# Kernel optimization log

Measured on AMD Instinct MI355X. Metric: run time of the kernel, lower is better.

The kernel has to match this reference:

```python
import jax, jax.numpy as jnp
import numpy as np

NUM_HEADS = 16
HEAD_DIM = 128  # d_out // num_heads
D_IN = 2048
D_OUT = 2048
B = 2
T = 2048
W_SCALE = 0.02  # keep softmax logits in a sane range


def setup_inputs() -> dict:
    key = jax.random.key(0)
    ks = jax.random.split(key, 6)
    x = jax.random.normal(ks[0], (B, T, D_IN), dtype=jnp.float32)
    Wq = jax.random.normal(ks[1], (D_OUT, D_IN), dtype=jnp.float32) * W_SCALE
    Wk = jax.random.normal(ks[2], (HEAD_DIM, D_IN), dtype=jnp.float32) * W_SCALE
    Wv = jax.random.normal(ks[3], (HEAD_DIM, D_IN), dtype=jnp.float32) * W_SCALE
    Wo = jax.random.normal(ks[4], (D_OUT, D_OUT), dtype=jnp.float32) * W_SCALE
    bo = jnp.zeros((D_OUT,), dtype=jnp.float32)
    return {"x": x, "Wq": Wq, "Wk": Wk, "Wv": Wv, "Wo": Wo, "bo": bo}


def reference(x, Wq, Wk, Wv, Wo, bo):
    b, t, _ = x.shape
    # projections (torch nn.Linear: y = x @ W.T)
    q = jnp.einsum('btd,ed->bte', x, Wq).reshape(b, t, NUM_HEADS, HEAD_DIM)
    q = q.transpose(0, 2, 1, 3)                      # [b, H, T, hd]
    k = jnp.einsum('btd,ed->bte', x, Wk)             # [b, T, hd] single KV head
    v = jnp.einsum('btd,ed->bte', x, Wv)             # [b, T, hd]
    # MQA: single K/V head broadcast across all query heads
    scale = 1.0 / jnp.sqrt(jnp.float32(HEAD_DIM))
    scores = jnp.einsum('bhqd,bkd->bhqk', q, k) * scale  # [b, H, T, T]
    # NOTE: the original module computes a causal mask but never applies it,
    # so attention is unmasked (faithful to source).
    w = jax.nn.softmax(scores, axis=-1)
    ctx = jnp.einsum('bhqk,bkd->bhqd', w, v)         # [b, H, T, hd]
    ctx = ctx.transpose(0, 2, 1, 3).reshape(b, t, D_OUT)
    return jnp.einsum('btd,ed->bte', ctx, Wo) + bo
```

## Files before the change

### kernel.cpp

```cpp
#include <hip/hip_runtime.h>

typedef unsigned short u16;
typedef unsigned int   u32;
typedef __bf16 bf16x8 __attribute__((ext_vector_type(8)));
typedef float  f32x4  __attribute__((ext_vector_type(4)));
typedef u32    u32x2  __attribute__((ext_vector_type(2)));

constexpr int TB   = 2;
constexpr int TT   = 2048;
constexpr int DIN  = 2048;
constexpr int DOUT = 2048;
constexpr int NH   = 16;
constexpr int HD   = 128;
constexpr int MR   = TB * TT;
constexpr int NQKV = DOUT + 2 * HD;

constexpr float QSC = 0.08838834764831845f * 1.4426950408889634f;

__device__ __forceinline__ u16 f2b(float f) {
  return __builtin_bit_cast(u16, (__bf16)f);
}

__global__ __launch_bounds__(256) void k_cast_all(const float* __restrict__ x,
                                                  const float* __restrict__ wq,
                                                  const float* __restrict__ wk,
                                                  const float* __restrict__ wv,
                                                  const float* __restrict__ wo,
                                                  u16* __restrict__ xb,
                                                  u16* __restrict__ wqkv,
                                                  u16* __restrict__ wob) {
  int bid = blockIdx.x;
  const float* s; u16* d; int base;
  if (bid < 8192)       { s = x;  d = xb;   base = bid; }
  else if (bid < 12288) { s = wq; d = wqkv; base = bid - 8192; }
  else if (bid < 12544) { s = wk; d = wqkv + (size_t)DOUT * DIN;        base = bid - 12288; }
  else if (bid < 12800) { s = wv; d = wqkv + (size_t)(DOUT + HD) * DIN; base = bid - 12544; }
  else                  { s = wo; d = wob;  base = bid - 12800; }
  int i = (base * 256 + threadIdx.x) * 4;
  float4 v = *(const float4*)(s + i);
  ushort4 o;
  o.x = f2b(v.x); o.y = f2b(v.y); o.z = f2b(v.z); o.w = f2b(v.w);
  *(ushort4*)(d + i) = o;
}

__device__ __forceinline__ void async16(const u16* g, u16* l) {
  __builtin_amdgcn_global_load_lds((const __attribute__((address_space(1))) void*)g,
                                   (__attribute__((address_space(3))) void*)l,
                                   16, 0, 0);
}

template<bool F32OUT>
__global__ __launch_bounds__(512) void k_gemm(const u16* __restrict__ A,
                                              const u16* __restrict__ Bm,
                                              void* __restrict__ Cv,
                                              const float* __restrict__ bias,
                                              int M, int N, int K) {
  __shared__ u16 lA[128 * 64];
  __shared__ u16 lB[128 * 64];
  const int tid = threadIdx.x;
  const int w = tid >> 6, l = tid & 63;
  const int wr = w >> 1, wc = w & 1;
  const int r16 = l & 15, kq = l >> 4;

  int nwg = gridDim.x * gridDim.y;
  int wg = blockIdx.y * gridDim.x + blockIdx.x;
  if ((nwg & 7) == 0) wg = (wg & 7) * (nwg >> 3) + (wg >> 3);
  const int rowS = (wg / gridDim.x) * 128, colS = (wg % gridDim.x) * 128;

  f32x4 acc[2][4] = {};

  for (int k0 = 0; k0 < K; k0 += 64) {
    __syncthreads();
#pragma unroll
    for (int i = 0; i < 2; ++i) {
      int e = i * 512 + tid;
      int row = e >> 3, col = (e & 7) * 8;
      async16(A  + (size_t)(rowS + row) * K + k0 + col, &lA[e * 8]);
      async16(Bm + (size_t)(colS + row) * K + k0 + col, &lB[e * 8]);
    }
    __syncthreads();
#pragma unroll
    for (int kk = 0; kk < 2; ++kk) {
      bf16x8 af[2], bfr[4];
#pragma unroll
      for (int m = 0; m < 2; ++m)
        af[m] = *(const bf16x8*)&lA[(wr * 32 + m * 16 + r16) * 64 + kk * 32 + kq * 8];
#pragma unroll
      for (int n = 0; n < 4; ++n)
        bfr[n] = *(const bf16x8*)&lB[(wc * 64 + n * 16 + r16) * 64 + kk * 32 + kq * 8];
      __builtin_amdgcn_s_setprio(1);
#pragma unroll
      for (int m = 0; m < 2; ++m)
#pragma unroll
        for (int n = 0; n < 4; ++n)
          acc[m][n] = __builtin_amdgcn_mfma_f32_16x16x32_bf16(af[m], bfr[n], acc[m][n], 0, 0, 0);
      __builtin_amdgcn_s_setprio(0);
    }
  }

#pragma unroll
  for (int m = 0; m < 2; ++m)
#pragma unroll
    for (int n = 0; n < 4; ++n)
#pragma unroll
      for (int j = 0; j < 4; ++j) {
        int r = rowS + wr * 32 + m * 16 + kq * 4 + j;
        int c = colS + wc * 64 + n * 16 + r16;
        if constexpr (F32OUT) {
          ((float*)Cv)[(size_t)r * N + c] = acc[m][n][j] + bias[c];
        } else {
          float v = acc[m][n][j];
          if (c < DOUT) v *= QSC;
          ((u16*)Cv)[(size_t)r * N + c] = f2b(v);
        }
      }
}

__global__ __launch_bounds__(256) void k_transpose_v(const u16* __restrict__ qkv,
                                                     u16* __restrict__ vtg) {
  __shared__ u16 tile[64 * 136];
  const int blk = blockIdx.x;
  const int b = blk / (TT / 64), t0 = (blk % (TT / 64)) * 64;
  const int tid = threadIdx.x;
#pragma unroll
  for (int i = 0; i < 4; ++i) {
    int e = i * 256 + tid;
    int row = e >> 4, col = (e & 15) * 8;
    *(uint4*)&tile[row * 136 + col] =
        *(const uint4*)(qkv + (size_t)(b * TT + t0 + row) * NQKV + DOUT + HD + col);
  }
  __syncthreads();
#pragma unroll
  for (int i = 0; i < 4; ++i) {
    int e = i * 256 + tid;
    int d = e >> 3, tc = (e & 7) * 8;
    u16 tmp[8];
#pragma unroll
    for (int j = 0; j < 8; ++j) tmp[j] = tile[(tc + j) * 136 + d];
    *(uint4*)(vtg + ((size_t)b * HD + d) * TT + t0 + tc) = *(uint4*)tmp;
  }
}

#define KT_IDX(r, c) ((r) * 128 + ((c) ^ (((r) & 7) << 3)))
#define VT_IDX(r, c) ((r) * 64 + ((c) ^ (((r) & 7) << 3)))

__global__ __launch_bounds__(512) void k_attn(const u16* __restrict__ qkv,
                                              const u16* __restrict__ vtg,
                                              u16* __restrict__ ctxg) {
  __shared__ u16 Kt[2][64 * 128];
  __shared__ u16 Vt[2][128 * 64];

  const int qt = blockIdx.x, h = blockIdx.y, b = blockIdx.z;
  const int tid = threadIdx.x, w = tid >> 6, l = tid & 63;
  const int r16 = l & 15, kq = l >> 4;
  const int q0 = qt * 128 + w * 16;
  const size_t rowbase = (size_t)b * TT;

  bf16x8 qf[4];
  const u16* qrow = qkv + (rowbase + q0 + r16) * NQKV + h * HD + kq * 8;
#pragma unroll
  for (int kk = 0; kk < 4; ++kk) qf[kk] = *(const bf16x8*)(qrow + kk * 32);

  const int krow0 = tid >> 4, kcol = (tid & 15) * 8;
  const int vrow0 = tid >> 3, vcol = (tid & 7) * 8;
  const u16* kglob = qkv + (rowbase)*NQKV + DOUT;
  const u16* vglob = vtg + (size_t)b * HD * TT;

  uint4 kr0, kr1, vr0, vr1;
  auto load_tiles = [&](int kv0) {
    const u16* kb = kglob + (size_t)kv0 * NQKV;
    kr0 = *(const uint4*)(kb + (size_t)krow0 * NQKV + kcol);
    kr1 = *(const uint4*)(kb + (size_t)(krow0 + 32) * NQKV + kcol);
    const u16* vb = vglob + kv0;
    vr0 = *(const uint4*)(vb + (size_t)vrow0 * TT + vcol);
    vr1 = *(const uint4*)(vb + (size_t)(vrow0 + 64) * TT + vcol);
  };
  auto write_tiles = [&](int buf) {
    *(uint4*)&Kt[buf][KT_IDX(krow0, kcol)]      = kr0;
    *(uint4*)&Kt[buf][KT_IDX(krow0 + 32, kcol)] = kr1;
    *(uint4*)&Vt[buf][VT_IDX(vrow0, vcol)]      = vr0;
    *(uint4*)&Vt[buf][VT_IDX(vrow0 + 64, vcol)] = vr1;
  };

  f32x4 ctx[8] = {};
  float l_run = 0.0f;

  load_tiles(0);
  write_tiles(0);
  __syncthreads();

  for (int t = 0; t < TT / 64; ++t) {
    const int cur = t & 1;
    if (t < TT / 64 - 1) load_tiles((t + 1) * 64);

    f32x4 s[4] = {};
#pragma unroll
    for (int n = 0; n < 4; ++n) {
      bf16x8 kf[4];
#pragma unroll
      for (int kk = 0; kk < 4; ++kk)
        kf[kk] = *(const bf16x8*)&Kt[cur][KT_IDX(n * 16 + r16, kk * 32 + kq * 8)];
      __builtin_amdgcn_s_setprio(1);
#pragma unroll
      for (int kk = 0; kk < 4; ++kk)
        s[n] = __builtin_amdgcn_mfma_f32_16x16x32_bf16(kf[kk], qf[kk], s[n], 0, 0, 0);
      __builtin_amdgcn_s_setprio(0);
    }

    float rsum = 0.0f;
    float p[4][4];
#pragma unroll
    for (int n = 0; n < 4; ++n)
#pragma unroll
      for (int j = 0; j < 4; ++j) {
        p[n][j] = exp2f(s[n][j]);
        rsum += p[n][j];
      }
    rsum += __shfl_xor(rsum, 16);
    rsum += __shfl_xor(rsum, 32);
    l_run += rsum;

    u32 pk[4][2];
#pragma unroll
    for (int n = 0; n < 4; ++n) {
      pk[n][0] = (u32)f2b(p[n][0]) | ((u32)f2b(p[n][1]) << 16);
      pk[n][1] = (u32)f2b(p[n][2]) | ((u32)f2b(p[n][3]) << 16);
    }

#pragma unroll
    for (int hh = 0; hh < 2; ++hh) {
      union { bf16x8 v; u32 wds[4]; } pu;
      pu.wds[0] = pk[2 * hh][0];     pu.wds[1] = pk[2 * hh][1];
      pu.wds[2] = pk[2 * hh + 1][0]; pu.wds[3] = pk[2 * hh + 1][1];
      __builtin_amdgcn_s_setprio(1);
#pragma unroll
      for (int f = 0; f < 8; ++f) {
        union { bf16x8 v; u32x2 half[2]; } vu;
        vu.half[0] = *(const u32x2*)&Vt[cur][VT_IDX(f * 16 + r16, (2 * hh) * 16 + kq * 4)];
        vu.half[1] = *(const u32x2*)&Vt[cur][VT_IDX(f * 16 + r16, (2 * hh + 1) * 16 + kq * 4)];
        ctx[f] = __builtin_amdgcn_mfma_f32_16x16x32_bf16(vu.v, pu.v, ctx[f], 0, 0, 0);
      }
      __builtin_amdgcn_s_setprio(0);
    }

    if (t < TT / 64 - 1) write_tiles(cur ^ 1);
    __syncthreads();
  }

  const float inv = 1.0f / l_run;
  u16* crow = ctxg + (rowbase + q0 + r16) * DOUT + h * HD + kq * 4;
#pragma unroll
  for (int f = 0; f < 8; ++f) {
    u32x2 o;
    o[0] = (u32)f2b(ctx[f][0] * inv) | ((u32)f2b(ctx[f][1] * inv) << 16);
    o[1] = (u32)f2b(ctx[f][2] * inv) | ((u32)f2b(ctx[f][3] * inv) << 16);
    *(u32x2*)(crow + f * 16) = o;
  }
}

extern "C" void kernel_launch(void* const* d_in, const int* in_sizes, int n_in,
                              void* d_out, int out_size, void* d_ws, size_t ws_size,
                              hipStream_t stream) {
  const float* x  = (const float*)d_in[0];
  const float* Wq = (const float*)d_in[1];
  const float* Wk = (const float*)d_in[2];
  const float* Wv = (const float*)d_in[3];
  const float* Wo = (const float*)d_in[4];
  const float* bo = (const float*)d_in[5];
  float* out = (float*)d_out;

  char* ws = (char*)d_ws;
  u16* xb   = (u16*)(ws + 0);
  u16* wqkv = (u16*)(ws + 16777216);
  u16* wo   = (u16*)(ws + 26214400);
  u16* qkv  = (u16*)(ws + 34603008);
  u16* vtg  = (u16*)(ws + 53477376);
  u16* ctx  = (u16*)(ws + 54525952);

  k_cast_all<<<16896, 256, 0, stream>>>(x, Wq, Wk, Wv, Wo, xb, wqkv, wo);

  k_gemm<false><<<dim3(NQKV / 128, MR / 128), 512, 0, stream>>>(
      xb, wqkv, (void*)qkv, nullptr, MR, NQKV, DIN);

  k_transpose_v<<<TB * TT / 64, 256, 0, stream>>>(qkv, vtg);

  k_attn<<<dim3(TT / 128, NH, TB), 512, 0, stream>>>(qkv, vtg, ctx);

  k_gemm<true><<<dim3(DOUT / 128, MR / 128), 512, 0, stream>>>(
      ctx, wo, (void*)out, bo, MR, DOUT, DOUT);
}
```

Measured before the change: 359.5 us.

## Double-buffer GEMM LDS tiles and stage softmax probabilities through LDS

The GEMM kernel now double-buffers its A/B LDS tiles, issuing async global-to-LDS loads for the next K-slice while MFMAs run on the current one. This removes the load-then-wait bubble of the single-buffer loop, at the cost of doubling GEMM LDS use (64KB), which may lower occupancy. In attention, each wave writes its P fragments to a small per-wave LDS scratch and reads them back in the contiguous K layout. That lets each V fragment be fetched as one 16-byte LDS read instead of two 8-byte ones. It relies on intra-wave ordering for the P scratch without an explicit barrier.

```diff
diff --git a/kernel.cpp b/kernel.cpp
--- a/kernel.cpp
+++ b/kernel.cpp
@@ -55,8 +55,8 @@
                                               void* __restrict__ Cv,
                                               const float* __restrict__ bias,
                                               int M, int N, int K) {
-  __shared__ u16 lA[128 * 64];
-  __shared__ u16 lB[128 * 64];
+  __shared__ u16 lA[2][128 * 64];
+  __shared__ u16 lB[2][128 * 64];
   const int tid = threadIdx.x;
   const int w = tid >> 6, l = tid & 63;
   const int wr = w >> 1, wc = w & 1;
@@ -67,27 +67,35 @@
   if ((nwg & 7) == 0) wg = (wg & 7) * (nwg >> 3) + (wg >> 3);
   const int rowS = (wg / gridDim.x) * 128, colS = (wg % gridDim.x) * 128;
 
-  f32x4 acc[2][4] = {};
-
-  for (int k0 = 0; k0 < K; k0 += 64) {
-    __syncthreads();
+  const int srow = tid >> 3, scol = (tid & 7) * 8;
+
+  auto stage = [&](int buf, int k0) {
 #pragma unroll
     for (int i = 0; i < 2; ++i) {
       int e = i * 512 + tid;
-      int row = e >> 3, col = (e & 7) * 8;
-      async16(A  + (size_t)(rowS + row) * K + k0 + col, &lA[e * 8]);
-      async16(Bm + (size_t)(colS + row) * K + k0 + col, &lB[e * 8]);
-    }
-    __syncthreads();
+      async16(A  + (size_t)(rowS + srow + i * 64) * K + k0 + scol, &lA[buf][e * 8]);
+      async16(Bm + (size_t)(colS + srow + i * 64) * K + k0 + scol, &lB[buf][e * 8]);
+    }
+  };
+
+  f32x4 acc[2][4] = {};
+
+  stage(0, 0);
+  asm volatile("s_waitcnt vmcnt(0)" ::: "memory");
+  __syncthreads();
+
+  int cur = 0;
+  for (int k0 = 0; k0 < K; k0 += 64) {
+    if (k0 + 64 < K) stage(cur ^ 1, k0 + 64);
 #pragma unroll
     for (int kk = 0; kk < 2; ++kk) {
       bf16x8 af[2], bfr[4];
 #pragma unroll
       for (int m = 0; m < 2; ++m)
-        af[m] = *(const bf16x8*)&lA[(wr * 32 + m * 16 + r16) * 64 + kk * 32 + kq * 8];
+        af[m] = *(const bf16x8*)&lA[cur][(wr * 32 + m * 16 + r16) * 64 + kk * 32 + kq * 8];
 #pragma unroll
       for (int n = 0; n < 4; ++n)
-        bfr[n] = *(const bf16x8*)&lB[(wc * 64 + n * 16 + r16) * 64 + kk * 32 + kq * 8];
+        bfr[n] = *(const bf16x8*)&lB[cur][(wc * 64 + n * 16 + r16) * 64 + kk * 32 + kq * 8];
       __builtin_amdgcn_s_setprio(1);
 #pragma unroll
       for (int m = 0; m < 2; ++m)
@@ -96,6 +104,9 @@
           acc[m][n] = __builtin_amdgcn_mfma_f32_16x16x32_bf16(af[m], bfr[n], acc[m][n], 0, 0, 0);
       __builtin_amdgcn_s_setprio(0);
     }
+    asm volatile("s_waitcnt vmcnt(0)" ::: "memory");
+    __syncthreads();
+    cur ^= 1;
   }
 
 #pragma unroll
@@ -149,6 +160,7 @@
                                               u16* __restrict__ ctxg) {
   __shared__ u16 Kt[2][64 * 128];
   __shared__ u16 Vt[2][128 * 64];
+  __shared__ u16 Pt[8][16 * 40];
 
   const int qt = blockIdx.x, h = blockIdx.y, b = blockIdx.z;
   const int tid = threadIdx.x, w = tid >> 6, l = tid & 63;
@@ -227,18 +239,20 @@
       pk[n][1] = (u32)f2b(p[n][2]) | ((u32)f2b(p[n][3]) << 16);
     }
 
+    u16* pw = Pt[w];
 #pragma unroll
     for (int hh = 0; hh < 2; ++hh) {
-      union { bf16x8 v; u32 wds[4]; } pu;
-      pu.wds[0] = pk[2 * hh][0];     pu.wds[1] = pk[2 * hh][1];
-      pu.wds[2] = pk[2 * hh + 1][0]; pu.wds[3] = pk[2 * hh + 1][1];
+      u32x2 w0, w1;
+      w0[0] = pk[2 * hh][0];     w0[1] = pk[2 * hh][1];
+      w1[0] = pk[2 * hh + 1][0]; w1[1] = pk[2 * hh + 1][1];
+      *(u32x2*)&pw[r16 * 40 + kq * 4]      = w0;
+      *(u32x2*)&pw[r16 * 40 + 16 + kq * 4] = w1;
+      bf16x8 pf = *(const bf16x8*)&pw[r16 * 40 + kq * 8];
       __builtin_amdgcn_s_setprio(1);
 #pragma unroll
       for (int f = 0; f < 8; ++f) {
-        union { bf16x8 v; u32x2 half[2]; } vu;
-        vu.half[0] = *(const u32x2*)&Vt[cur][VT_IDX(f * 16 + r16, (2 * hh) * 16 + kq * 4)];
-        vu.half[1] = *(const u32x2*)&Vt[cur][VT_IDX(f * 16 + r16, (2 * hh + 1) * 16 + kq * 4)];
-        ctx[f] = __builtin_amdgcn_mfma_f32_16x16x32_bf16(vu.v, pu.v, ctx[f], 0, 0, 0);
+        bf16x8 vf = *(const bf16x8*)&Vt[cur][VT_IDX(f * 16 + r16, hh * 32 + kq * 8)];
+        ctx[f] = __builtin_amdgcn_mfma_f32_16x16x32_bf16(vf, pf, ctx[f], 0, 0, 0);
       }
       __builtin_amdgcn_s_setprio(0);
     }
```

Result: faster. 346.5 us (-3.6%).
